# Kernel optimization log

Measured on AMD Instinct MI355X. Metric: run time of the kernel, lower is better.

The kernel has to match this reference:

```python
import jax, jax.numpy as jnp
import numpy as np
import math

EMBED = 1024
HEADS = 16
HEAD_DIM = EMBED // HEADS
FFN = 4 * EMBED
LAYERS = 3
SEQ = 2048
BATCH = 2
INPUT_DIM = 64


def make_pe(max_len, d_model):
    pe = np.zeros((max_len, d_model), dtype=np.float32)
    pos = np.arange(max_len, dtype=np.float32)[:, None]
    div = np.exp(np.arange(0, d_model, 2, dtype=np.float32) * (-math.log(10000.0) / d_model))
    pe[:, 0::2] = np.sin(pos * div)
    pe[:, 1::2] = np.cos(pos * div)
    return jnp.asarray(pe)


def setup_inputs() -> dict:
    key = jax.random.key(0)
    ks = jax.random.split(key, 16)
    s = lambda k, shape, fan: jax.random.normal(k, shape, dtype=jnp.float32) / np.sqrt(fan)
    return {
        "x": jax.random.normal(ks[0], (BATCH, SEQ, INPUT_DIM), dtype=jnp.float32),
        "mask": jnp.ones((BATCH, 1, 1, SEQ), dtype=bool),
        "embed_W": s(ks[1], (INPUT_DIM, EMBED), INPUT_DIM),
        "embed_b": jnp.zeros((EMBED,), jnp.float32),
        "pe": make_pe(SEQ, EMBED),
        "Wq": s(ks[2], (LAYERS, HEAD_DIM, HEAD_DIM), HEAD_DIM),
        "Wk": s(ks[3], (LAYERS, HEAD_DIM, HEAD_DIM), HEAD_DIM),
        "Wv": s(ks[4], (LAYERS, HEAD_DIM, HEAD_DIM), HEAD_DIM),
        "Wo": s(ks[5], (LAYERS, EMBED, EMBED), EMBED),
        "bo": jnp.zeros((LAYERS, EMBED), jnp.float32),
        "ln1_g": jnp.ones((LAYERS, EMBED), jnp.float32),
        "ln1_b": jnp.zeros((LAYERS, EMBED), jnp.float32),
        "W1": s(ks[6], (LAYERS, EMBED, FFN), EMBED),
        "b1": jnp.zeros((LAYERS, FFN), jnp.float32),
        "W2": s(ks[7], (LAYERS, FFN, EMBED), FFN),
        "b2": jnp.zeros((LAYERS, EMBED), jnp.float32),
        "ln2_g": jnp.ones((LAYERS, EMBED), jnp.float32),
        "ln2_b": jnp.zeros((LAYERS, EMBED), jnp.float32),
    }


def _layernorm(x, g, b, eps=1e-5):
    mu = jnp.mean(x, axis=-1, keepdims=True)
    var = jnp.var(x, axis=-1, keepdims=True)
    return (x - mu) * jax.lax.rsqrt(var + eps) * g + b


def reference(x, mask, embed_W, embed_b, pe, Wq, Wk, Wv, Wo, bo,
              ln1_g, ln1_b, W1, b1, W2, b2, ln2_g, ln2_b):
    N, S, _ = x.shape
    scale = 1.0 / np.sqrt(EMBED).astype(np.float32)  # note: sqrt(embed_size), as in original
    h = x @ embed_W + embed_b + pe[None, :S, :]
    for l in range(LAYERS):
        hr = h.reshape(N, S, HEADS, HEAD_DIM)
        q = jnp.einsum('nshd,de->nshe', hr, Wq[l])
        k = jnp.einsum('nshd,de->nshe', hr, Wk[l])
        v = jnp.einsum('nshd,de->nshe', hr, Wv[l])
        energy = jnp.einsum('nqhd,nkhd->nhqk', q, k)  # (N,H,S,S)
        energy = jnp.where(mask == 0, jnp.float32(-1e20), energy)
        attn = jax.nn.softmax(energy * scale, axis=-1)
        o = jnp.einsum('nhqk,nkhd->nqhd', attn, v).reshape(N, S, EMBED)
        o = o @ Wo[l] + bo[l]
        x1 = _layernorm(o + h, ln1_g[l], ln1_b[l])
        ff = jax.nn.relu(x1 @ W1[l] + b1[l]) @ W2[l] + b2[l]
        h = _layernorm(ff + x1, ln2_g[l], ln2_b[l])
    return h
```

## Files before the change

### kernel.cpp

```cpp
#include <hip/hip_runtime.h>


typedef __attribute__((ext_vector_type(8))) unsigned short us8;
typedef __attribute__((ext_vector_type(4))) unsigned short us4;
typedef __attribute__((ext_vector_type(8))) __bf16 bf16x8;
typedef __attribute__((ext_vector_type(4))) float f32x4;

#define SEQ   2048
#define HEADS 16
#define HD    64
#define EMB   1024
#define FFN_  4096
#define NBAT  2
#define ROWS  (NBAT*SEQ)

__device__ __forceinline__ float bf2f(unsigned short s) {
    return __builtin_bit_cast(float, ((unsigned int)s) << 16);
}
__device__ __forceinline__ unsigned short f2bf(float f) {
    unsigned int u = __builtin_bit_cast(unsigned int, f);
    u += 0x7fffu + ((u >> 16) & 1u);
    return (unsigned short)(u >> 16);
}
__device__ __forceinline__ bf16x8 ldfrag(const unsigned short* p) {
    us8 v = *(const us8*)p;
    return __builtin_bit_cast(bf16x8, v);
}
__device__ __forceinline__ us8 cvt8(const float* p) {
    float4 f0 = *(const float4*)p, f1 = *(const float4*)(p + 4);
    us8 v;
    v[0] = f2bf(f0.x); v[1] = f2bf(f0.y); v[2] = f2bf(f0.z); v[3] = f2bf(f0.w);
    v[4] = f2bf(f1.x); v[5] = f2bf(f1.y); v[6] = f2bf(f1.z); v[7] = f2bf(f1.w);
    return v;
}
__device__ __forceinline__ void async_cp16(const unsigned short* g, unsigned short* l) {
    __builtin_amdgcn_global_load_lds(
        (const __attribute__((address_space(1))) void*)g,
        (__attribute__((address_space(3))) void*)l, 16, 0, 0);
}

__device__ __forceinline__ void transpose_tile(
    const float* __restrict__ W, unsigned short* __restrict__ Wt,
    int K, int N, int k0, int n0, int t)
{
    __shared__ float T[64][65];
    const int kk = t >> 4, nn = (t & 15) * 4;
#pragma unroll
    for (int r = 0; r < 4; r++) {
        float4 v = *(const float4*)(W + (size_t)(k0 + kk + r*16)*N + n0 + nn);
        T[kk + r*16][nn+0] = v.x; T[kk + r*16][nn+1] = v.y;
        T[kk + r*16][nn+2] = v.z; T[kk + r*16][nn+3] = v.w;
    }
    __syncthreads();
    const int n = t >> 2, kc = (t & 3) * 16;
    us8 a, b;
#pragma unroll
    for (int i = 0; i < 8; i++) a[i] = f2bf(T[kc + i][n]);
#pragma unroll
    for (int i = 0; i < 8; i++) b[i] = f2bf(T[kc + 8 + i][n]);
    *(us8*)(Wt + (size_t)(n0 + n)*K + k0 + kc)     = a;
    *(us8*)(Wt + (size_t)(n0 + n)*K + k0 + kc + 8) = b;
}

__global__ __launch_bounds__(256) void wprep(
    const float* __restrict__ W, unsigned short* __restrict__ Wt,
    const int K, const int N)
{
    transpose_tile(W, Wt, K, N, blockIdx.x*64, blockIdx.y*64, threadIdx.x);
}

__global__ __launch_bounds__(256) void wprep_qkv(
    const float* __restrict__ Wq, const float* __restrict__ Wk,
    const float* __restrict__ Wv, unsigned short* __restrict__ Wt3)
{
    const float* W = blockIdx.z == 0 ? Wq : (blockIdx.z == 1 ? Wk : Wv);
    transpose_tile(W, Wt3 + (size_t)blockIdx.z*64*64, 64, 64, 0, 0, threadIdx.x);
}

__global__ __launch_bounds__(256) void cvt_bf16(
    const float* __restrict__ src, unsigned short* __restrict__ dst, const int n8)
{
    int i = blockIdx.x*256 + threadIdx.x;
    if (i < n8) *(us8*)(dst + (size_t)i*8) = cvt8(src + (size_t)i*8);
}

__global__ __launch_bounds__(256) void vtrans(
    const unsigned short* __restrict__ QKV, unsigned short* __restrict__ Vt)
{
    __shared__ __align__(16) unsigned short T[64*72];
    const int s0 = blockIdx.x*64, h = blockIdx.y, n = blockIdx.z;
    const int t = threadIdx.x;
    const int s = t & 63, c16 = (t >> 6) * 16;
    const unsigned short* src =
        QKV + ((size_t)(n*SEQ + s0 + s)*HEADS + h)*192 + 128 + c16;
    *(us8*)&T[s*72 + c16]     = *(const us8*)(src);
    *(us8*)&T[s*72 + c16 + 8] = *(const us8*)(src + 8);
    __syncthreads();
    const int f = t & 63, r16 = (t >> 6) * 16;
    us8 a, b;
#pragma unroll
    for (int i = 0; i < 8; i++) a[i] = T[(r16 + i)*72 + f];
#pragma unroll
    for (int i = 0; i < 8; i++) b[i] = T[(r16 + 8 + i)*72 + f];
    unsigned short* dst = Vt + ((size_t)(n*HEADS + h)*HD + f)*SEQ + s0 + r16;
    *(us8*)dst       = a;
    *(us8*)(dst + 8) = b;
}

template<int BM, int BN, int WR, int WC>
__global__ __launch_bounds__(WR*WC*64) void gemm_bt(
    const unsigned short* __restrict__ A, const unsigned short* __restrict__ Bt,
    void* __restrict__ Cout, const int out_bf16,
    const float* __restrict__ bias, const float* __restrict__ pe,
    const int M, const int N, const int K, const int relu)
{
    constexpr int BK  = 32;
    constexpr int NW  = WR*WC;
    constexpr int MF  = BM/(WR*16);
    constexpr int NF  = BN/(WC*16);
    constexpr int ACH = BM*4;
    constexpr int BCH = BN*4;
    constexpr int APW = ACH/NW;
    constexpr int BPW = BCH/NW;
    __shared__ __align__(16) unsigned short As[BM*BK];
    __shared__ __align__(16) unsigned short Bs[BN*BK];

    const int tid  = threadIdx.x;
    const int lane = tid & 63;
    const int wave = tid >> 6;
    const int wm   = (wave / WC) * (BM/WR);
    const int wn   = (wave % WC) * (BN/WC);
    const int bm   = blockIdx.x * BM;
    const int bn   = blockIdx.y * BN;
    const int m15  = lane & 15;
    const int quad = lane >> 4;

    f32x4 acc[MF][NF];
#pragma unroll
    for (int i = 0; i < MF; i++)
#pragma unroll
        for (int j = 0; j < NF; j++) acc[i][j] = (f32x4){0.f, 0.f, 0.f, 0.f};

    for (int kt = 0; kt < K; kt += BK) {
#pragma unroll
        for (int j = 0; j < APW/64; j++) {
            const int c = wave*APW + j*64 + lane;
            async_cp16(A + (size_t)(bm + (c >> 2))*K + kt + (c & 3)*8,
                       As + (size_t)(wave*APW + j*64)*8);
        }
#pragma unroll
        for (int j = 0; j < BPW/64; j++) {
            const int c = wave*BPW + j*64 + lane;
            async_cp16(Bt + (size_t)(bn + (c >> 2))*K + kt + (c & 3)*8,
                       Bs + (size_t)(wave*BPW + j*64)*8);
        }
        __syncthreads();

        bf16x8 af[MF], bfr[NF];
#pragma unroll
        for (int i = 0; i < MF; i++) af[i]  = ldfrag(&As[(wm + i*16 + m15)*BK + quad*8]);
#pragma unroll
        for (int j = 0; j < NF; j++) bfr[j] = ldfrag(&Bs[(wn + j*16 + m15)*BK + quad*8]);
#pragma unroll
        for (int i = 0; i < MF; i++)
#pragma unroll
            for (int j = 0; j < NF; j++)
                acc[i][j] = __builtin_amdgcn_mfma_f32_16x16x32_bf16(af[i], bfr[j], acc[i][j], 0, 0, 0);
        __syncthreads();
    }

#pragma unroll
    for (int i = 0; i < MF; i++) {
#pragma unroll
        for (int j = 0; j < NF; j++) {
#pragma unroll
            for (int r = 0; r < 4; r++) {
                int row = bm + wm + i*16 + quad*4 + r;
                int col = bn + wn + j*16 + m15;
                float v = acc[i][j][r];
                if (bias) v += bias[col];
                if (pe)   v += pe[(size_t)(row & (SEQ-1))*EMB + col];
                if (relu) v = fmaxf(v, 0.f);
                if (out_bf16) ((unsigned short*)Cout)[(size_t)row*N + col] = f2bf(v);
                else          ((float*)Cout)[(size_t)row*N + col] = v;
            }
        }
    }
}

__global__ __launch_bounds__(256) void flash_attn(
    const unsigned short* __restrict__ QKV, const unsigned short* __restrict__ Vt,
    unsigned short* __restrict__ O)
{
    const int h = blockIdx.y, n = blockIdx.z;
    const int tid = threadIdx.x, lane = tid & 63, wave = tid >> 6;
    const int m15 = lane & 15, quad = lane >> 4;
    const int q0 = blockIdx.x*128 + wave*32;

    __shared__ __align__(16) unsigned short Ks[64*64];
    __shared__ __align__(16) unsigned short Vs[64*64];
    __shared__ __align__(16) unsigned short Pl[4][32*36];

    bf16x8 aq[2][2];
#pragma unroll
    for (int mi = 0; mi < 2; mi++) {
        const unsigned short* qp =
            QKV + ((size_t)(n*SEQ + q0 + mi*16 + m15)*HEADS + h)*192;
        aq[mi][0] = ldfrag(qp + quad*8);
        aq[mi][1] = ldfrag(qp + 32 + quad*8);
    }

    f32x4 accO[2][4];
    f32x4 lacc[2];
#pragma unroll
    for (int mi = 0; mi < 2; mi++) {
        lacc[mi] = (f32x4){0.f, 0.f, 0.f, 0.f};
#pragma unroll
        for (int ft = 0; ft < 4; ft++) accO[mi][ft] = (f32x4){0.f, 0.f, 0.f, 0.f};
    }

    const float sl2e = 0.03125f * 1.4426950408889634f;
    const unsigned short* kb = QKV + ((size_t)(n*SEQ)*HEADS + h)*192 + 64;
    const unsigned short* vb = Vt + (size_t)(n*HEADS + h)*HD*SEQ;

    us8 ones_u;
#pragma unroll
    for (int i = 0; i < 8; i++) ones_u[i] = 0x3F80;
    const bf16x8 ones = __builtin_bit_cast(bf16x8, ones_u);

    const int r0  = tid >> 3;
    const int r1  = r0 + 32;
    const int sc  = ((tid & 7) ^ (r0 & 7)) * 8;
    const int swz = (m15 & 7);

    for (int kt = 0; kt < SEQ; kt += 64) {
        async_cp16(kb + (size_t)(kt + r0)*(HEADS*192) + sc, Ks + (size_t)(wave*64)*8);
        async_cp16(kb + (size_t)(kt + r1)*(HEADS*192) + sc, Ks + (size_t)(256 + wave*64)*8);
        async_cp16(vb + (size_t)r0*SEQ + kt + sc,           Vs + (size_t)(wave*64)*8);
        async_cp16(vb + (size_t)r1*SEQ + kt + sc,           Vs + (size_t)(256 + wave*64)*8);
        __syncthreads();

#pragma unroll
        for (int s2 = 0; s2 < 2; s2++) {
            bf16x8 ck[2][2], cv[4];
#pragma unroll
            for (int nt = 0; nt < 2; nt++)
#pragma unroll
                for (int ks = 0; ks < 2; ks++) {
                    const int kk = s2*32 + nt*16 + m15;
                    ck[nt][ks] = ldfrag(&Ks[kk*64 + (((ks*4 + quad) ^ swz) * 8)]);
                }
#pragma unroll
            for (int ft = 0; ft < 4; ft++) {
                const int d = ft*16 + m15;
                cv[ft] = ldfrag(&Vs[d*64 + (((s2*4 + quad) ^ swz) * 8)]);
            }

            f32x4 sv[2][2];
            __builtin_amdgcn_s_setprio(1);
#pragma unroll
            for (int mi = 0; mi < 2; mi++)
#pragma unroll
                for (int nt = 0; nt < 2; nt++) {
                    f32x4 z = (f32x4){0.f, 0.f, 0.f, 0.f};
                    z = __builtin_amdgcn_mfma_f32_16x16x32_bf16(aq[mi][0], ck[nt][0], z, 0, 0, 0);
                    z = __builtin_amdgcn_mfma_f32_16x16x32_bf16(aq[mi][1], ck[nt][1], z, 0, 0, 0);
                    sv[mi][nt] = z;
                }
            __builtin_amdgcn_s_setprio(0);

#pragma unroll
            for (int mi = 0; mi < 2; mi++)
#pragma unroll
                for (int nt = 0; nt < 2; nt++)
#pragma unroll
                    for (int r = 0; r < 4; r++) {
                        float p = exp2f(fminf(sv[mi][nt][r] * sl2e, 80.f));
                        Pl[wave][(mi*16 + quad*4 + r)*36 + nt*16 + m15] = f2bf(p);
                    }

            bf16x8 pf[2];
#pragma unroll
            for (int mi = 0; mi < 2; mi++)
                pf[mi] = ldfrag(&Pl[wave][(mi*16 + m15)*36 + quad*8]);
            __builtin_amdgcn_s_setprio(1);
#pragma unroll
            for (int mi = 0; mi < 2; mi++) {
#pragma unroll
                for (int ft = 0; ft < 4; ft++)
                    accO[mi][ft] = __builtin_amdgcn_mfma_f32_16x16x32_bf16(
                        pf[mi], cv[ft], accO[mi][ft], 0, 0, 0);
                lacc[mi] = __builtin_amdgcn_mfma_f32_16x16x32_bf16(
                    pf[mi], ones, lacc[mi], 0, 0, 0);
            }
            __builtin_amdgcn_s_setprio(0);
        }
        __syncthreads();
    }

#pragma unroll
    for (int mi = 0; mi < 2; mi++)
#pragma unroll
        for (int r = 0; r < 4; r++) {
            const float inv = 1.0f / lacc[mi][r];
            const int row = q0 + mi*16 + quad*4 + r;
#pragma unroll
            for (int ft = 0; ft < 4; ft++)
                O[((size_t)(n*SEQ + row)*HEADS + h)*HD + ft*16 + m15] =
                    f2bf(accO[mi][ft][r] * inv);
        }
}

__global__ __launch_bounds__(256) void add_ln_kernel(
    const unsigned short* __restrict__ a, const unsigned short* __restrict__ res,
    const float* __restrict__ g, const float* __restrict__ b,
    void* __restrict__ out, const int out_fp32)
{
    const int row = blockIdx.x;
    const int tid = threadIdx.x;
    const int c0  = tid * 4;

    us4 va = *(const us4*)(a   + (size_t)row*EMB + c0);
    us4 vr = *(const us4*)(res + (size_t)row*EMB + c0);
    float x[4];
#pragma unroll
    for (int i = 0; i < 4; i++) x[i] = bf2f(va[i]) + bf2f(vr[i]);

    float s = x[0] + x[1] + x[2] + x[3];
    float q = x[0]*x[0] + x[1]*x[1] + x[2]*x[2] + x[3]*x[3];
#pragma unroll
    for (int off = 1; off < 64; off <<= 1) {
        s += __shfl_xor(s, off, 64);
        q += __shfl_xor(q, off, 64);
    }
    __shared__ float rs[4], rq[4];
    if ((tid & 63) == 0) { rs[tid >> 6] = s; rq[tid >> 6] = q; }
    __syncthreads();
    s = rs[0] + rs[1] + rs[2] + rs[3];
    q = rq[0] + rq[1] + rq[2] + rq[3];

    const float mu   = s * (1.0f/EMB);
    const float var  = q * (1.0f/EMB) - mu*mu;
    const float rstd = rsqrtf(var + 1e-5f);

    float4 vg = *(const float4*)(g + c0);
    float4 vb = *(const float4*)(b + c0);
    float y0 = (x[0] - mu) * rstd * vg.x + vb.x;
    float y1 = (x[1] - mu) * rstd * vg.y + vb.y;
    float y2 = (x[2] - mu) * rstd * vg.z + vb.z;
    float y3 = (x[3] - mu) * rstd * vg.w + vb.w;

    if (out_fp32) {
        *(float4*)((float*)out + (size_t)row*EMB + c0) = (float4){y0, y1, y2, y3};
    } else {
        us4 o;
        o[0] = f2bf(y0); o[1] = f2bf(y1); o[2] = f2bf(y2); o[3] = f2bf(y3);
        *(us4*)((unsigned short*)out + (size_t)row*EMB + c0) = o;
    }
}

extern "C" void kernel_launch(void* const* d_in, const int* in_sizes, int n_in,
                              void* d_out, int out_size, void* d_ws, size_t ws_size,
                              hipStream_t stream)
{
    (void)in_sizes; (void)n_in; (void)out_size; (void)ws_size;
    const float* x    = (const float*)d_in[0];
    const float* embW = (const float*)d_in[2];
    const float* embB = (const float*)d_in[3];
    const float* pe   = (const float*)d_in[4];
    const float* Wq   = (const float*)d_in[5];
    const float* Wk   = (const float*)d_in[6];
    const float* Wv   = (const float*)d_in[7];
    const float* Wo   = (const float*)d_in[8];
    const float* bo   = (const float*)d_in[9];
    const float* ln1g = (const float*)d_in[10];
    const float* ln1b = (const float*)d_in[11];
    const float* W1   = (const float*)d_in[12];
    const float* b1   = (const float*)d_in[13];
    const float* W2   = (const float*)d_in[14];
    const float* b2   = (const float*)d_in[15];
    const float* ln2g = (const float*)d_in[16];
    const float* ln2b = (const float*)d_in[17];

    char* ws = (char*)d_ws;
    const size_t MB = 1024*1024;
    unsigned short* qkv = (unsigned short*)ws;
    unsigned short* ff  = (unsigned short*)ws;
    unsigned short* vt  = (unsigned short*)(ws + 24*MB);
    unsigned short* t   = (unsigned short*)(ws + 32*MB);
    unsigned short* h   = (unsigned short*)(ws + 40*MB);
    unsigned short* x1  = (unsigned short*)(ws + 48*MB);
    unsigned short* wx  = (unsigned short*)(ws + 56*MB);
    unsigned short* xb    = t;
    unsigned short* embWt = t + 256*1024;
    unsigned short* qkvWt = t;
    unsigned short* o   = (unsigned short*)d_out;

    cvt_bf16<<<128, 256, 0, stream>>>(x, xb, ROWS*64/8);
    wprep<<<dim3(1, EMB/64), 256, 0, stream>>>(embW, embWt, 64, EMB);
    gemm_bt<128,64,4,1><<<dim3(ROWS/128, EMB/64), 256, 0, stream>>>(
        xb, embWt, h, 1, embB, pe, ROWS, EMB, 64, 0);

    for (int l = 0; l < 3; l++) {
        wprep_qkv<<<dim3(1,1,3), 256, 0, stream>>>(
            Wq + (size_t)l*HD*HD, Wk + (size_t)l*HD*HD, Wv + (size_t)l*HD*HD, qkvWt);
        gemm_bt<256,64,4,1><<<dim3(ROWS*HEADS/256, 3), 256, 0, stream>>>(
            h, qkvWt, qkv, 1, nullptr, nullptr, ROWS*HEADS, 192, HD, 0);

        vtrans<<<dim3(SEQ/64, HEADS, NBAT), 256, 0, stream>>>(qkv, vt);
        flash_attn<<<dim3(SEQ/128, HEADS, NBAT), 256, 0, stream>>>(qkv, vt, o);

        wprep<<<dim3(EMB/64, EMB/64), 256, 0, stream>>>(
            Wo + (size_t)l*EMB*EMB, wx, EMB, EMB);
        gemm_bt<128,64,4,1><<<dim3(ROWS/128, EMB/64), 256, 0, stream>>>(
            o, wx, t, 1, bo + (size_t)l*EMB, nullptr, ROWS, EMB, EMB, 0);
        add_ln_kernel<<<ROWS, 256, 0, stream>>>(
            t, h, ln1g + (size_t)l*EMB, ln1b + (size_t)l*EMB, x1, 0);

        wprep<<<dim3(EMB/64, FFN_/64), 256, 0, stream>>>(
            W1 + (size_t)l*EMB*FFN_, wx, EMB, FFN_);
        gemm_bt<128,128,2,2><<<dim3(ROWS/128, FFN_/128), 256, 0, stream>>>(
            x1, wx, ff, 1, b1 + (size_t)l*FFN_, nullptr, ROWS, FFN_, EMB, 1);
        wprep<<<dim3(FFN_/64, EMB/64), 256, 0, stream>>>(
            W2 + (size_t)l*FFN_*EMB, wx, FFN_, EMB);
        gemm_bt<128,64,4,1><<<dim3(ROWS/128, EMB/64), 256, 0, stream>>>(
            ff, wx, t, 1, b2 + (size_t)l*EMB, nullptr, ROWS, EMB, FFN_, 0);

        if (l == 2)
            add_ln_kernel<<<ROWS, 256, 0, stream>>>(
                t, x1, ln2g + (size_t)l*EMB, ln2b + (size_t)l*EMB, d_out, 1);
        else
            add_ln_kernel<<<ROWS, 256, 0, stream>>>(
                t, x1, ln2g + (size_t)l*EMB, ln2b + (size_t)l*EMB, h, 0);
    }
}
```

Measured before the change: 1.147 ms.

## Double-buffer K/V tiles in flash attention and pack P with hardware bf16 convert

The flash attention loop now stages the next 64-key K and V tile into a second LDS buffer before computing on the current one. The goal is to overlap global-to-LDS copies with the MFMA and exp work instead of stalling at a barrier each iteration. The softmax probabilities are also converted two at a time with v_cvt_pk_bf16_f32, replacing the software round-to-nearest bf16 conversion. The cost is doubled K/V LDS use, which may lower occupancy, and a redundant wrapped prefetch on the final iteration.

```diff
diff --git a/kernel.cpp b/kernel.cpp
--- a/kernel.cpp
+++ b/kernel.cpp
@@ -197,8 +197,8 @@
     const int m15 = lane & 15, quad = lane >> 4;
     const int q0 = blockIdx.x*128 + wave*32;
 
-    __shared__ __align__(16) unsigned short Ks[64*64];
-    __shared__ __align__(16) unsigned short Vs[64*64];
+    __shared__ __align__(16) unsigned short Ks[2][64*64];
+    __shared__ __align__(16) unsigned short Vs[2][64*64];
     __shared__ __align__(16) unsigned short Pl[4][32*36];
 
     bf16x8 aq[2][2];
@@ -233,12 +233,21 @@
     const int sc  = ((tid & 7) ^ (r0 & 7)) * 8;
     const int swz = (m15 & 7);
 
+    auto stage = [&](int buf, int kt) {
+        async_cp16(kb + (size_t)(kt + r0)*(HEADS*192) + sc, Ks[buf] + (size_t)(wave*64)*8);
+        async_cp16(kb + (size_t)(kt + r1)*(HEADS*192) + sc, Ks[buf] + (size_t)(256 + wave*64)*8);
+        async_cp16(vb + (size_t)r0*SEQ + kt + sc,           Vs[buf] + (size_t)(wave*64)*8);
+        async_cp16(vb + (size_t)r1*SEQ + kt + sc,           Vs[buf] + (size_t)(256 + wave*64)*8);
+    };
+
+    stage(0, 0);
+    __syncthreads();
+    int cur = 0;
+
     for (int kt = 0; kt < SEQ; kt += 64) {
-        async_cp16(kb + (size_t)(kt + r0)*(HEADS*192) + sc, Ks + (size_t)(wave*64)*8);
-        async_cp16(kb + (size_t)(kt + r1)*(HEADS*192) + sc, Ks + (size_t)(256 + wave*64)*8);
-        async_cp16(vb + (size_t)r0*SEQ + kt + sc,           Vs + (size_t)(wave*64)*8);
-        async_cp16(vb + (size_t)r1*SEQ + kt + sc,           Vs + (size_t)(256 + wave*64)*8);
-        __syncthreads();
+        stage(cur ^ 1, (kt + 64) & (SEQ - 1));
+        const unsigned short* ksp = Ks[cur];
+        const unsigned short* vsp = Vs[cur];
 
 #pragma unroll
         for (int s2 = 0; s2 < 2; s2++) {
@@ -248,12 +257,12 @@
 #pragma unroll
                 for (int ks = 0; ks < 2; ks++) {
                     const int kk = s2*32 + nt*16 + m15;
-                    ck[nt][ks] = ldfrag(&Ks[kk*64 + (((ks*4 + quad) ^ swz) * 8)]);
+                    ck[nt][ks] = ldfrag(&ksp[kk*64 + (((ks*4 + quad) ^ swz) * 8)]);
                 }
 #pragma unroll
             for (int ft = 0; ft < 4; ft++) {
                 const int d = ft*16 + m15;
-                cv[ft] = ldfrag(&Vs[d*64 + (((s2*4 + quad) ^ swz) * 8)]);
+                cv[ft] = ldfrag(&vsp[d*64 + (((s2*4 + quad) ^ swz) * 8)]);
             }
 
             f32x4 sv[2][2];
@@ -274,9 +283,16 @@
 #pragma unroll
                 for (int nt = 0; nt < 2; nt++)
 #pragma unroll
-                    for (int r = 0; r < 4; r++) {
-                        float p = exp2f(fminf(sv[mi][nt][r] * sl2e, 80.f));
-                        Pl[wave][(mi*16 + quad*4 + r)*36 + nt*16 + m15] = f2bf(p);
+                    for (int r = 0; r < 4; r += 2) {
+                        float p0 = exp2f(fminf(sv[mi][nt][r]   * sl2e, 80.f));
+                        float p1 = exp2f(fminf(sv[mi][nt][r+1] * sl2e, 80.f));
+                        unsigned int pk;
+                        asm("v_cvt_pk_bf16_f32 %0, %1, %2"
+                            : "=v"(pk) : "v"(p0), "v"(p1));
+                        Pl[wave][(mi*16 + quad*4 + r    )*36 + nt*16 + m15] =
+                            (unsigned short)(pk & 0xffffu);
+                        Pl[wave][(mi*16 + quad*4 + r + 1)*36 + nt*16 + m15] =
+                            (unsigned short)(pk >> 16);
                     }
 
             bf16x8 pf[2];
@@ -295,7 +311,9 @@
             }
             __builtin_amdgcn_s_setprio(0);
         }
+
         __syncthreads();
+        cur ^= 1;
     }
 
 #pragma unroll
```

Result: no change. 1.130 ms (-1.4%).
